# Kernel tuning notes

Hardware: AMD Instinct MI355X
Metric: run time of the kernel (lower is better)

The kernel has to match this reference:

```python
import jax, jax.numpy as jnp
import numpy as np

S, N, H = 4096, 32, 512

def setup_inputs() -> dict:
    key = jax.random.key(0)
    ks = jax.random.split(key, 8)
    scale = 1.0 / np.sqrt(H)
    return {
        "hidden": jax.random.normal(ks[0], (N, H), dtype=jnp.float32),
        "encoder_outputs": jax.random.normal(ks[1], (S, N, H), dtype=jnp.float32),
        "W_w": jax.random.uniform(ks[2], (H, H), jnp.float32, -scale, scale),
        "W_b": jax.random.uniform(ks[3], (H,), jnp.float32, -scale, scale),
        "U_w": jax.random.uniform(ks[4], (H, H), jnp.float32, -scale, scale),
        "U_b": jax.random.uniform(ks[5], (H,), jnp.float32, -scale, scale),
        "v_w": jax.random.uniform(ks[6], (1, H), jnp.float32, -scale, scale),
        "v_b": jax.random.uniform(ks[7], (1,), jnp.float32, -scale, scale),
    }

def reference(hidden, encoder_outputs, W_w, W_b, U_w, U_b, v_w, v_b):
    # W(hidden): [N,H] -> broadcast over seq dim (equivalent to expand then Linear)
    wh = hidden @ W_w.T + W_b                      # [N, H]
    ue = jnp.einsum('snh,kh->snk', encoder_outputs, U_w) + U_b  # [S, N, H]
    energy = jnp.tanh(wh[None, :, :] + ue)         # [S, N, H]
    score = jnp.einsum('snh,oh->sno', energy, v_w) + v_b        # [S, N, 1]
    attention_weights = jax.nn.softmax(score, axis=0)           # softmax over seq
    context = jnp.sum(attention_weights * encoder_outputs, axis=0)  # [N, H]
    return (context, attention_weights)
```

## Files before the change

kernel.cpp:

```cpp
#include <hip/hip_runtime.h>
#include <hip/hip_bf16.h>

#define Sdim 4096
#define Ndim 32
#define Hdim 512
#define Mdim (Sdim * Ndim)

#define BM 128
#define BN 256
#define BK 64

typedef __bf16 bf16x8 __attribute__((ext_vector_type(8)));
typedef float f32x4 __attribute__((ext_vector_type(4)));
typedef unsigned short ushort8v __attribute__((ext_vector_type(8)));

__device__ __forceinline__ void load_lds16(const void* g, void* l) {
    __builtin_amdgcn_global_load_lds(
        (const __attribute__((address_space(1))) void*)g,
        (__attribute__((address_space(3))) void*)l, 16, 0, 0);
}

__device__ __forceinline__ float ftanh(float x) {
    float e = __expf(2.f * x);
    return 1.f - 2.f / (e + 1.f);
}

__global__ __launch_bounds__(256) void k_prep_bias(
    const float* __restrict__ hidden, const float* __restrict__ Ww,
    const float* __restrict__ Wb, const float* __restrict__ Ubias,
    float* __restrict__ bias) {
    const int t = threadIdx.x, w = t >> 6, lane = t & 63;
    const int cc = blockIdx.x * 4 + w;
    const float4 w0 = *(const float4*)(Ww + (size_t)cc * Hdim + lane * 8);
    const float4 w1 = *(const float4*)(Ww + (size_t)cc * Hdim + lane * 8 + 4);
    const float wb = Wb[cc] + Ubias[cc];
    for (int n = 0; n < Ndim; ++n) {
        const float4 h0 = *(const float4*)(hidden + n * Hdim + lane * 8);
        const float4 h1 = *(const float4*)(hidden + n * Hdim + lane * 8 + 4);
        float p = w0.x * h0.x + w0.y * h0.y + w0.z * h0.z + w0.w * h0.w +
                  w1.x * h1.x + w1.y * h1.y + w1.z * h1.z + w1.w * h1.w;
        p += __shfl_xor(p, 1);  p += __shfl_xor(p, 2);
        p += __shfl_xor(p, 4);  p += __shfl_xor(p, 8);
        p += __shfl_xor(p, 16); p += __shfl_xor(p, 32);
        if (lane == 0) bias[n * Hdim + cc] = p + wb;
    }
}

__global__ __launch_bounds__(256) void k_cvt(
    const float* __restrict__ src, unsigned short* __restrict__ dst) {
    const int i = blockIdx.x * 256 + threadIdx.x;
    float4 v = ((const float4*)src)[i];
    union { __hip_bfloat162 h[2]; ushort4 u; } r;
    r.h[0] = __float22bfloat162_rn(make_float2(v.x, v.y));
    r.h[1] = __float22bfloat162_rn(make_float2(v.z, v.w));
    ((ushort4*)dst)[i] = r.u;
}

__global__ __launch_bounds__(512, 4) void k_gemm_score(
    const float* __restrict__ enc,
    const unsigned short* __restrict__ Ub,
    const float* __restrict__ bias,
    const float* __restrict__ vw,
    float* __restrict__ scorep) {
    __shared__ __align__(16) unsigned short Asm[BM][72];
    __shared__ __align__(16) unsigned short Bsm[BN * BK];
    __shared__ float ssm[4][BM];

    const int t = threadIdx.x;
    const int lane = t & 63;
    const int w = t >> 6;
    const int wM = w >> 2;
    const int wN = w & 3;
    const int c = lane & 15;
    const int q = lane >> 4;

    const int rowblk = blockIdx.x >> 1;
    const int colblk = blockIdx.x & 1;
    const int mBase = rowblk * BM;
    const int colBase = colblk * BN;

    const int ar = t >> 2;
    const int aq = t & 3;
    const int asw = ((ar >> 3) & 1) << 1;
    const float4* arow =
        (const float4*)(enc + (size_t)(mBase + ar) * Hdim) + aq * 4;
    unsigned short* awr = &Asm[ar][((2 * aq) ^ asw) * 8];

    const int coff = lane >> 3;
    const int bch = (lane & 7) ^ coff;
    const unsigned short* bsrc =
        Ub + (size_t)(colBase + w * 8 + coff) * Hdim + bch * 8;
    unsigned short* bdst = Bsm + (w * 8) * BK;

    const int sA = ((c >> 3) & 1) << 1;
    const int sB = c & 7;

    f32x4 acc[4][4];
#pragma unroll
    for (int i = 0; i < 4; ++i)
#pragma unroll
        for (int j = 0; j < 4; ++j) acc[i][j] = (f32x4){0.f, 0.f, 0.f, 0.f};

    float4 a0 = arow[0], a1 = arow[1], a2 = arow[2], a3 = arow[3];

#pragma unroll 1
    for (int kk = 0; kk < Hdim / BK; ++kk) {
        asm volatile("" ::: "memory");
        __builtin_amdgcn_s_barrier();
        asm volatile("" ::: "memory");
        __builtin_amdgcn_sched_barrier(0);

#pragma unroll
        for (int g = 0; g < 4; ++g)
            load_lds16(bsrc + (size_t)g * 64 * Hdim + kk * BK,
                       bdst + g * 64 * BK);
        asm volatile("" ::: "memory");
        __builtin_amdgcn_sched_barrier(0);

        union { __hip_bfloat162 h[4]; ushort8v v; } p0, p1;
        p0.h[0] = __float22bfloat162_rn(make_float2(a0.x, a0.y));
        p0.h[1] = __float22bfloat162_rn(make_float2(a0.z, a0.w));
        p0.h[2] = __float22bfloat162_rn(make_float2(a1.x, a1.y));
        p0.h[3] = __float22bfloat162_rn(make_float2(a1.z, a1.w));
        p1.h[0] = __float22bfloat162_rn(make_float2(a2.x, a2.y));
        p1.h[1] = __float22bfloat162_rn(make_float2(a2.z, a2.w));
        p1.h[2] = __float22bfloat162_rn(make_float2(a3.x, a3.y));
        p1.h[3] = __float22bfloat162_rn(make_float2(a3.z, a3.w));
        *(ushort8v*)awr = p0.v;
        *(ushort8v*)(awr + 8) = p1.v;

        const int kn = (kk < Hdim / BK - 1) ? kk + 1 : kk;
        const float4* ap = arow + kn * 16;
        a0 = ap[0]; a1 = ap[1]; a2 = ap[2]; a3 = ap[3];

        asm volatile("" ::: "memory");
        __builtin_amdgcn_sched_barrier(0);
        asm volatile("s_waitcnt vmcnt(4) lgkmcnt(0)" ::: "memory");
        __builtin_amdgcn_s_barrier();
        asm volatile("" ::: "memory");
        __builtin_amdgcn_sched_barrier(0);

#pragma unroll 1
        for (int h = 0; h < 2; ++h) {
            bf16x8 af[4], bfr[4];
#pragma unroll
            for (int mi = 0; mi < 4; ++mi) {
                const int row = wM * 64 + mi * 16 + c;
                af[mi] =
                    *(const bf16x8*)&Asm[row][(((h << 2) | q) ^ sA) * 8];
            }
#pragma unroll
            for (int ni = 0; ni < 4; ++ni) {
                const int lc = wN * 64 + ni * 16 + c;
                bfr[ni] = *(const bf16x8*)&Bsm[lc * BK +
                                               (((h << 2) | q) ^ sB) * 8];
            }
#pragma unroll
            for (int mi = 0; mi < 4; ++mi)
#pragma unroll
                for (int ni = 0; ni < 4; ++ni)
                    acc[mi][ni] = __builtin_amdgcn_mfma_f32_16x16x32_bf16(
                        af[mi], bfr[ni], acc[mi][ni], 0, 0, 0);
        }
    }
    asm volatile("" :: "v"(a0.x), "v"(a1.x), "v"(a2.x), "v"(a3.x));

    float vcol[4];
#pragma unroll
    for (int ni = 0; ni < 4; ++ni)
        vcol[ni] = vw[colBase + wN * 64 + ni * 16 + c];

#pragma unroll
    for (int mi = 0; mi < 4; ++mi) {
#pragma unroll
        for (int reg = 0; reg < 4; ++reg) {
            const int rl = wM * 64 + mi * 16 + q * 4 + reg;
            const int n = rl & 31;
            float p = 0.f;
#pragma unroll
            for (int ni = 0; ni < 4; ++ni) {
                const int col = colBase + wN * 64 + ni * 16 + c;
                float e = acc[mi][ni][reg] + bias[n * Hdim + col];
                p += vcol[ni] * ftanh(e);
            }
            p += __shfl_xor(p, 1);
            p += __shfl_xor(p, 2);
            p += __shfl_xor(p, 4);
            p += __shfl_xor(p, 8);
            if (c == 0) ssm[wN][rl] = p;
        }
    }
    __syncthreads();
    if (t < BM) {
        const int m = mBase + t;
        const float s = ssm[0][t] + ssm[1][t] + ssm[2][t] + ssm[3][t];
        scorep[colblk * Mdim + (m & 31) * Sdim + (m >> 5)] = s;
    }
}

__global__ __launch_bounds__(256) void k_softmax(
    const float* __restrict__ scorep,
    float* __restrict__ out_w) {
    const int n = blockIdx.x;
    const int t = threadIdx.x;
    const int w = t >> 6;
    __shared__ float row[Sdim];
    __shared__ float red[8];
    const float4* s0 = (const float4*)(scorep + n * Sdim);
    const float4* s1 = (const float4*)(scorep + Mdim + n * Sdim);

    float mx = -1e30f;
    for (int i = t; i < Sdim / 4; i += 256) {
        float4 a = s0[i], b = s1[i];
        float4 v;
        v.x = a.x + b.x; v.y = a.y + b.y; v.z = a.z + b.z; v.w = a.w + b.w;
        ((float4*)row)[i] = v;
        mx = fmaxf(mx, fmaxf(fmaxf(v.x, v.y), fmaxf(v.z, v.w)));
    }
#pragma unroll
    for (int o = 32; o > 0; o >>= 1) mx = fmaxf(mx, __shfl_xor(mx, o));
    if ((t & 63) == 0) red[w] = mx;
    __syncthreads();
    mx = fmaxf(fmaxf(red[0], red[1]), fmaxf(red[2], red[3]));

    float sum = 0.f;
    for (int i = t; i < Sdim; i += 256) sum += __expf(row[i] - mx);
#pragma unroll
    for (int o = 32; o > 0; o >>= 1) sum += __shfl_xor(sum, o);
    if ((t & 63) == 0) red[4 + w] = sum;
    __syncthreads();
    sum = red[4] + red[5] + red[6] + red[7];
    const float inv = 1.f / sum;
    for (int i = t; i < Sdim; i += 256)
        out_w[i * Ndim + n] = __expf(row[i] - mx) * inv;
}

__global__ __launch_bounds__(512) void k_context(
    const float* __restrict__ enc, const float* __restrict__ wts,
    float* __restrict__ part) {
    const int n = blockIdx.x & 31;
    const int sc = blockIdx.x >> 5;
    const int s0 = sc * 256;
    const int t = threadIdx.x;
    const int g = t >> 6;
    const int lane = t & 63;
    const int h0 = lane * 8;
    float4 c0 = {0.f, 0.f, 0.f, 0.f}, c1 = {0.f, 0.f, 0.f, 0.f};
#pragma unroll 4
    for (int it = 0; it < 32; ++it) {
        const int s = s0 + it * 8 + g;
        const float wv = wts[(size_t)s * Ndim + n];
        const float* e = enc + ((size_t)s * Ndim + n) * Hdim + h0;
        const float4 e0 = *(const float4*)e;
        const float4 e1 = *(const float4*)(e + 4);
        c0.x += wv * e0.x; c0.y += wv * e0.y;
        c0.z += wv * e0.z; c0.w += wv * e0.w;
        c1.x += wv * e1.x; c1.y += wv * e1.y;
        c1.z += wv * e1.z; c1.w += wv * e1.w;
    }
    __shared__ __align__(16) float4 red[7][128];
    if (g > 0) { red[g - 1][lane * 2] = c0; red[g - 1][lane * 2 + 1] = c1; }
    __syncthreads();
    if (g == 0) {
#pragma unroll
        for (int i = 0; i < 7; ++i) {
            const float4 b0 = red[i][lane * 2];
            const float4 b1 = red[i][lane * 2 + 1];
            c0.x += b0.x; c0.y += b0.y; c0.z += b0.z; c0.w += b0.w;
            c1.x += b1.x; c1.y += b1.y; c1.z += b1.z; c1.w += b1.w;
        }
        float* o = part + (size_t)(sc * 32 + n) * Hdim + h0;
        *(float4*)o = c0;
        *(float4*)(o + 4) = c1;
    }
}

__global__ __launch_bounds__(256) void k_ctx_reduce(
    const float* __restrict__ part, float* __restrict__ out) {
    const int j = blockIdx.x * 256 + threadIdx.x;
    float4 s = {0.f, 0.f, 0.f, 0.f};
    for (int i = 0; i < 16; ++i) {
        const float4 v = ((const float4*)part)[i * 4096 + j];
        s.x += v.x; s.y += v.y; s.z += v.z; s.w += v.w;
    }
    ((float4*)out)[j] = s;
}

extern "C" void kernel_launch(void* const* d_in, const int* in_sizes, int n_in,
                              void* d_out, int out_size, void* d_ws,
                              size_t ws_size, hipStream_t stream) {
    const float* hidden = (const float*)d_in[0];
    const float* enc    = (const float*)d_in[1];
    const float* Ww     = (const float*)d_in[2];
    const float* Wb     = (const float*)d_in[3];
    const float* Uw     = (const float*)d_in[4];
    const float* Ubias  = (const float*)d_in[5];
    const float* vw     = (const float*)d_in[6];

    float* out = (float*)d_out;

    char* ws = (char*)d_ws;
    float* bias          = (float*)(ws);
    unsigned short* Ub16 = (unsigned short*)(ws + (64 << 10));
    float* scorep        = (float*)(ws + (576 << 10));
    float* part          = (float*)(ws + (64 << 10));

    k_prep_bias<<<128, 256, 0, stream>>>(hidden, Ww, Wb, Ubias, bias);
    k_cvt<<<256, 256, 0, stream>>>(Uw, Ub16);
    k_gemm_score<<<(Mdim / BM) * 2, 512, 0, stream>>>(enc, Ub16, bias, vw,
                                                      scorep);
    k_softmax<<<Ndim, 256, 0, stream>>>(scorep, out + Ndim * Hdim);
    k_context<<<Ndim * (Sdim / 256), 512, 0, stream>>>(enc, out + Ndim * Hdim,
                                                       part);
    k_ctx_reduce<<<16, 256, 0, stream>>>(part, out);
}
```

Before: 483.1 us.

## Use full-width GEMM tiles and fuse softmax normalization into context kernel

The score GEMM now uses 64x512 tiles so each block covers all output columns. The A operand (fp32 encoder rows) is therefore read and converted once instead of twice, and the two partial-score buffers disappear. A0/A1 prefetch is double-buffered two k-steps ahead. Softmax is split: a small kernel computes 1/sum(exp(score)) with no max subtraction, and the context kernel computes and writes the normalized weights itself before the weighted sum. Dropping the max subtraction risks overflow if scores are large, and the larger B tile increases LDS use, which may reduce occupancy.

Result: slower. 495.6 us (+2.6%).

```diff
diff --git a/kernel.cpp b/kernel.cpp
--- a/kernel.cpp
+++ b/kernel.cpp
@@ -6,8 +6,8 @@
 #define Hdim 512
 #define Mdim (Sdim * Ndim)
 
-#define BM 128
-#define BN 256
+#define BM 64
+#define BN 512
 #define BK 64
 
 typedef __bf16 bf16x8 __attribute__((ext_vector_type(8)));
@@ -56,6 +56,49 @@
     ((ushort4*)dst)[i] = r.u;
 }
 
+#define GS_STEP(KK, A0, A1)                                                    \
+    {                                                                          \
+        asm volatile("" ::: "memory");                                         \
+        __builtin_amdgcn_s_barrier();                                          \
+        asm volatile("" ::: "memory");                                         \
+        __builtin_amdgcn_sched_barrier(0);                                     \
+        _Pragma("unroll") for (int g = 0; g < 8; ++g)                          \
+            load_lds16(bsrc + (size_t)g * 8 * Hdim + (KK)*BK,                  \
+                       bdst + g * 8 * BK);                                     \
+        asm volatile("" ::: "memory");                                         \
+        __builtin_amdgcn_sched_barrier(0);                                     \
+        union { __hip_bfloat162 h[4]; ushort8v v; } pk;                        \
+        pk.h[0] = __float22bfloat162_rn(make_float2(A0.x, A0.y));              \
+        pk.h[1] = __float22bfloat162_rn(make_float2(A0.z, A0.w));              \
+        pk.h[2] = __float22bfloat162_rn(make_float2(A1.x, A1.y));              \
+        pk.h[3] = __float22bfloat162_rn(make_float2(A1.z, A1.w));              \
+        *(ushort8v*)awr = pk.v;                                                \
+        {                                                                      \
+            const int kn = ((KK) + 2 < 8) ? (KK) + 2 : 7;                      \
+            A0 = *(const float4*)(abase + kn * 64);                            \
+            A1 = *(const float4*)(abase + kn * 64 + 4);                        \
+        }                                                                      \
+        asm volatile("" ::: "memory");                                         \
+        __builtin_amdgcn_sched_barrier(0);                                     \
+        asm volatile("s_waitcnt vmcnt(2) lgkmcnt(0)" ::: "memory");            \
+        __builtin_amdgcn_s_barrier();                                          \
+        asm volatile("" ::: "memory");                                         \
+        __builtin_amdgcn_sched_barrier(0);                                     \
+        _Pragma("unroll 1") for (int h = 0; h < 2; ++h) {                      \
+            bf16x8 af[4], bfr[4];                                              \
+            const int ch = (h << 2) | q;                                       \
+            _Pragma("unroll") for (int mi = 0; mi < 4; ++mi)                   \
+                af[mi] = *(const bf16x8*)&Asm[mi * 16 + c][ch * 8];            \
+            _Pragma("unroll") for (int ni = 0; ni < 4; ++ni)                   \
+                bfr[ni] = *(const bf16x8*)&Bsm[(w * 64 + ni * 16 + c) * BK +   \
+                                               ((ch ^ sB) * 8)];               \
+            _Pragma("unroll") for (int mi = 0; mi < 4; ++mi)                   \
+                _Pragma("unroll") for (int ni = 0; ni < 4; ++ni)               \
+                    acc[mi][ni] = __builtin_amdgcn_mfma_f32_16x16x32_bf16(     \
+                        af[mi], bfr[ni], acc[mi][ni], 0, 0, 0);                \
+        }                                                                      \
+    }
+
 __global__ __launch_bounds__(512, 4) void k_gemm_score(
     const float* __restrict__ enc,
     const unsigned short* __restrict__ Ub,
@@ -64,35 +107,24 @@
     float* __restrict__ scorep) {
     __shared__ __align__(16) unsigned short Asm[BM][72];
     __shared__ __align__(16) unsigned short Bsm[BN * BK];
-    __shared__ float ssm[4][BM];
+    __shared__ float ssm[8][BM];
 
     const int t = threadIdx.x;
     const int lane = t & 63;
     const int w = t >> 6;
-    const int wM = w >> 2;
-    const int wN = w & 3;
     const int c = lane & 15;
     const int q = lane >> 4;
 
-    const int rowblk = blockIdx.x >> 1;
-    const int colblk = blockIdx.x & 1;
-    const int mBase = rowblk * BM;
-    const int colBase = colblk * BN;
-
-    const int ar = t >> 2;
-    const int aq = t & 3;
-    const int asw = ((ar >> 3) & 1) << 1;
-    const float4* arow =
-        (const float4*)(enc + (size_t)(mBase + ar) * Hdim) + aq * 4;
-    unsigned short* awr = &Asm[ar][((2 * aq) ^ asw) * 8];
-
-    const int coff = lane >> 3;
-    const int bch = (lane & 7) ^ coff;
-    const unsigned short* bsrc =
-        Ub + (size_t)(colBase + w * 8 + coff) * Hdim + bch * 8;
-    unsigned short* bdst = Bsm + (w * 8) * BK;
-
-    const int sA = ((c >> 3) & 1) << 1;
+    const int mBase = blockIdx.x * BM;
+
+    const float* abase = enc + (size_t)(mBase + (t >> 3)) * Hdim + (t & 7) * 8;
+    unsigned short* awr = &Asm[t >> 3][(t & 7) * 8];
+
+    const int csub = lane >> 3;
+    const unsigned short* bsrc = Ub + (size_t)(w * 64 + csub) * Hdim +
+                                 ((lane & 7) ^ csub) * 8;
+    unsigned short* bdst = Bsm + (w * 64) * BK;
+
     const int sB = c & 7;
 
     f32x4 acc[4][4];
@@ -101,85 +133,32 @@
 #pragma unroll
         for (int j = 0; j < 4; ++j) acc[i][j] = (f32x4){0.f, 0.f, 0.f, 0.f};
 
-    float4 a0 = arow[0], a1 = arow[1], a2 = arow[2], a3 = arow[3];
+    float4 aA0 = *(const float4*)(abase + 0);
+    float4 aA1 = *(const float4*)(abase + 4);
+    float4 aB0 = *(const float4*)(abase + 64);
+    float4 aB1 = *(const float4*)(abase + 68);
 
 #pragma unroll 1
-    for (int kk = 0; kk < Hdim / BK; ++kk) {
-        asm volatile("" ::: "memory");
-        __builtin_amdgcn_s_barrier();
-        asm volatile("" ::: "memory");
-        __builtin_amdgcn_sched_barrier(0);
-
-#pragma unroll
-        for (int g = 0; g < 4; ++g)
-            load_lds16(bsrc + (size_t)g * 64 * Hdim + kk * BK,
-                       bdst + g * 64 * BK);
-        asm volatile("" ::: "memory");
-        __builtin_amdgcn_sched_barrier(0);
-
-        union { __hip_bfloat162 h[4]; ushort8v v; } p0, p1;
-        p0.h[0] = __float22bfloat162_rn(make_float2(a0.x, a0.y));
-        p0.h[1] = __float22bfloat162_rn(make_float2(a0.z, a0.w));
-        p0.h[2] = __float22bfloat162_rn(make_float2(a1.x, a1.y));
-        p0.h[3] = __float22bfloat162_rn(make_float2(a1.z, a1.w));
-        p1.h[0] = __float22bfloat162_rn(make_float2(a2.x, a2.y));
-        p1.h[1] = __float22bfloat162_rn(make_float2(a2.z, a2.w));
-        p1.h[2] = __float22bfloat162_rn(make_float2(a3.x, a3.y));
-        p1.h[3] = __float22bfloat162_rn(make_float2(a3.z, a3.w));
-        *(ushort8v*)awr = p0.v;
-        *(ushort8v*)(awr + 8) = p1.v;
-
-        const int kn = (kk < Hdim / BK - 1) ? kk + 1 : kk;
-        const float4* ap = arow + kn * 16;
-        a0 = ap[0]; a1 = ap[1]; a2 = ap[2]; a3 = ap[3];
-
-        asm volatile("" ::: "memory");
-        __builtin_amdgcn_sched_barrier(0);
-        asm volatile("s_waitcnt vmcnt(4) lgkmcnt(0)" ::: "memory");
-        __builtin_amdgcn_s_barrier();
-        asm volatile("" ::: "memory");
-        __builtin_amdgcn_sched_barrier(0);
-
-#pragma unroll 1
-        for (int h = 0; h < 2; ++h) {
-            bf16x8 af[4], bfr[4];
-#pragma unroll
-            for (int mi = 0; mi < 4; ++mi) {
-                const int row = wM * 64 + mi * 16 + c;
-                af[mi] =
-                    *(const bf16x8*)&Asm[row][(((h << 2) | q) ^ sA) * 8];
-            }
-#pragma unroll
-            for (int ni = 0; ni < 4; ++ni) {
-                const int lc = wN * 64 + ni * 16 + c;
-                bfr[ni] = *(const bf16x8*)&Bsm[lc * BK +
-                                               (((h << 2) | q) ^ sB) * 8];
-            }
-#pragma unroll
-            for (int mi = 0; mi < 4; ++mi)
-#pragma unroll
-                for (int ni = 0; ni < 4; ++ni)
-                    acc[mi][ni] = __builtin_amdgcn_mfma_f32_16x16x32_bf16(
-                        af[mi], bfr[ni], acc[mi][ni], 0, 0, 0);
-        }
-    }
-    asm volatile("" :: "v"(a0.x), "v"(a1.x), "v"(a2.x), "v"(a3.x));
+    for (int kk = 0; kk < 8; kk += 2) {
+        GS_STEP(kk, aA0, aA1);
+        GS_STEP(kk + 1, aB0, aB1);
+    }
+    asm volatile("" :: "v"(aA0.x), "v"(aA1.x), "v"(aB0.x), "v"(aB1.x));
 
     float vcol[4];
 #pragma unroll
-    for (int ni = 0; ni < 4; ++ni)
-        vcol[ni] = vw[colBase + wN * 64 + ni * 16 + c];
+    for (int ni = 0; ni < 4; ++ni) vcol[ni] = vw[w * 64 + ni * 16 + c];
 
 #pragma unroll
     for (int mi = 0; mi < 4; ++mi) {
 #pragma unroll
         for (int reg = 0; reg < 4; ++reg) {
-            const int rl = wM * 64 + mi * 16 + q * 4 + reg;
+            const int rl = mi * 16 + q * 4 + reg;
             const int n = rl & 31;
             float p = 0.f;
 #pragma unroll
             for (int ni = 0; ni < 4; ++ni) {
-                const int col = colBase + wN * 64 + ni * 16 + c;
+                const int col = w * 64 + ni * 16 + c;
                 float e = acc[mi][ni][reg] + bias[n * Hdim + col];
                 p += vcol[ni] * ftanh(e);
             }
@@ -187,56 +166,41 @@
             p += __shfl_xor(p, 2);
             p += __shfl_xor(p, 4);
             p += __shfl_xor(p, 8);
-            if (c == 0) ssm[wN][rl] = p;
+            if (c == 0) ssm[w][rl] = p;
         }
     }
     __syncthreads();
     if (t < BM) {
         const int m = mBase + t;
-        const float s = ssm[0][t] + ssm[1][t] + ssm[2][t] + ssm[3][t];
-        scorep[colblk * Mdim + (m & 31) * Sdim + (m >> 5)] = s;
-    }
-}
-
-__global__ __launch_bounds__(256) void k_softmax(
+        const float s = ssm[0][t] + ssm[1][t] + ssm[2][t] + ssm[3][t] +
+                        ssm[4][t] + ssm[5][t] + ssm[6][t] + ssm[7][t];
+        scorep[(m & 31) * Sdim + (m >> 5)] = s;
+    }
+}
+
+__global__ __launch_bounds__(256) void k_sumexp(
     const float* __restrict__ scorep,
-    float* __restrict__ out_w) {
+    float* __restrict__ sums) {
     const int n = blockIdx.x;
     const int t = threadIdx.x;
     const int w = t >> 6;
-    __shared__ float row[Sdim];
-    __shared__ float red[8];
-    const float4* s0 = (const float4*)(scorep + n * Sdim);
-    const float4* s1 = (const float4*)(scorep + Mdim + n * Sdim);
-
-    float mx = -1e30f;
+    const float4* p = (const float4*)(scorep + n * Sdim);
+    float s = 0.f;
     for (int i = t; i < Sdim / 4; i += 256) {
-        float4 a = s0[i], b = s1[i];
-        float4 v;
-        v.x = a.x + b.x; v.y = a.y + b.y; v.z = a.z + b.z; v.w = a.w + b.w;
-        ((float4*)row)[i] = v;
-        mx = fmaxf(mx, fmaxf(fmaxf(v.x, v.y), fmaxf(v.z, v.w)));
-    }
-#pragma unroll
-    for (int o = 32; o > 0; o >>= 1) mx = fmaxf(mx, __shfl_xor(mx, o));
-    if ((t & 63) == 0) red[w] = mx;
-    __syncthreads();
-    mx = fmaxf(fmaxf(red[0], red[1]), fmaxf(red[2], red[3]));
-
-    float sum = 0.f;
-    for (int i = t; i < Sdim; i += 256) sum += __expf(row[i] - mx);
-#pragma unroll
-    for (int o = 32; o > 0; o >>= 1) sum += __shfl_xor(sum, o);
-    if ((t & 63) == 0) red[4 + w] = sum;
-    __syncthreads();
-    sum = red[4] + red[5] + red[6] + red[7];
-    const float inv = 1.f / sum;
-    for (int i = t; i < Sdim; i += 256)
-        out_w[i * Ndim + n] = __expf(row[i] - mx) * inv;
+        const float4 v = p[i];
+        s += __expf(v.x) + __expf(v.y) + __expf(v.z) + __expf(v.w);
+    }
+#pragma unroll
+    for (int o = 32; o > 0; o >>= 1) s += __shfl_xor(s, o);
+    __shared__ float red[4];
+    if ((t & 63) == 0) red[w] = s;
+    __syncthreads();
+    if (t == 0) sums[n] = 1.f / (red[0] + red[1] + red[2] + red[3]);
 }
 
 __global__ __launch_bounds__(512) void k_context(
-    const float* __restrict__ enc, const float* __restrict__ wts,
+    const float* __restrict__ enc, const float* __restrict__ scorep,
+    const float* __restrict__ sums, float* __restrict__ out_w,
     float* __restrict__ part) {
     const int n = blockIdx.x & 31;
     const int sc = blockIdx.x >> 5;
@@ -245,11 +209,21 @@
     const int g = t >> 6;
     const int lane = t & 63;
     const int h0 = lane * 8;
+
+    __shared__ float wsm[256];
+    if (t < 256) {
+        const int s = s0 + t;
+        const float wv = __expf(scorep[n * Sdim + s]) * sums[n];
+        wsm[t] = wv;
+        out_w[(size_t)s * Ndim + n] = wv;
+    }
+    __syncthreads();
+
     float4 c0 = {0.f, 0.f, 0.f, 0.f}, c1 = {0.f, 0.f, 0.f, 0.f};
 #pragma unroll 4
     for (int it = 0; it < 32; ++it) {
         const int s = s0 + it * 8 + g;
-        const float wv = wts[(size_t)s * Ndim + n];
+        const float wv = wsm[it * 8 + g];
         const float* e = enc + ((size_t)s * Ndim + n) * Hdim + h0;
         const float4 e0 = *(const float4*)e;
         const float4 e1 = *(const float4*)(e + 4);
@@ -303,14 +277,14 @@
     float* bias          = (float*)(ws);
     unsigned short* Ub16 = (unsigned short*)(ws + (64 << 10));
     float* scorep        = (float*)(ws + (576 << 10));
-    float* part          = (float*)(ws + (64 << 10));
+    float* sums          = (float*)(ws + (1088 << 10));
+    float* part          = (float*)(ws + (1152 << 10));
 
     k_prep_bias<<<128, 256, 0, stream>>>(hidden, Ww, Wb, Ubias, bias);
     k_cvt<<<256, 256, 0, stream>>>(Uw, Ub16);
-    k_gemm_score<<<(Mdim / BM) * 2, 512, 0, stream>>>(enc, Ub16, bias, vw,
-                                                      scorep);
-    k_softmax<<<Ndim, 256, 0, stream>>>(scorep, out + Ndim * Hdim);
-    k_context<<<Ndim * (Sdim / 256), 512, 0, stream>>>(enc, out + Ndim * Hdim,
-                                                       part);
+    k_gemm_score<<<Mdim / BM, 512, 0, stream>>>(enc, Ub16, bias, vw, scorep);
+    k_sumexp<<<Ndim, 256, 0, stream>>>(scorep, sums);
+    k_context<<<Ndim * (Sdim / 256), 512, 0, stream>>>(enc, scorep, sums,
+                                                       out + Ndim * Hdim, part);
     k_ctx_reduce<<<16, 256, 0, stream>>>(part, out);
 }
```

## Merge prep kernels and fuse softmax normalization into context kernel

Applied to the files above, without the earlier changes.

Merges the bias precompute and weight conversion into one launch. Replaces the softmax kernel with a lighter sum-of-exponentials kernel and moves the final weight computation into the context kernel, which now writes the attention weights itself and uses half-size sequence chunks for more blocks. The max subtraction is dropped, which relies on scores staying small enough not to overflow the exponential. The partial-sum buffer doubles and the reduction loops over 32 partials.

Result: no change. 483.6 us (+0.1%).

```diff
diff --git a/kernel.cpp b/kernel.cpp
--- a/kernel.cpp
+++ b/kernel.cpp
@@ -25,35 +25,38 @@
     return 1.f - 2.f / (e + 1.f);
 }
 
-__global__ __launch_bounds__(256) void k_prep_bias(
+__global__ __launch_bounds__(256) void k_prep(
     const float* __restrict__ hidden, const float* __restrict__ Ww,
     const float* __restrict__ Wb, const float* __restrict__ Ubias,
-    float* __restrict__ bias) {
-    const int t = threadIdx.x, w = t >> 6, lane = t & 63;
-    const int cc = blockIdx.x * 4 + w;
-    const float4 w0 = *(const float4*)(Ww + (size_t)cc * Hdim + lane * 8);
-    const float4 w1 = *(const float4*)(Ww + (size_t)cc * Hdim + lane * 8 + 4);
-    const float wb = Wb[cc] + Ubias[cc];
-    for (int n = 0; n < Ndim; ++n) {
-        const float4 h0 = *(const float4*)(hidden + n * Hdim + lane * 8);
-        const float4 h1 = *(const float4*)(hidden + n * Hdim + lane * 8 + 4);
-        float p = w0.x * h0.x + w0.y * h0.y + w0.z * h0.z + w0.w * h0.w +
-                  w1.x * h1.x + w1.y * h1.y + w1.z * h1.z + w1.w * h1.w;
-        p += __shfl_xor(p, 1);  p += __shfl_xor(p, 2);
-        p += __shfl_xor(p, 4);  p += __shfl_xor(p, 8);
-        p += __shfl_xor(p, 16); p += __shfl_xor(p, 32);
-        if (lane == 0) bias[n * Hdim + cc] = p + wb;
-    }
-}
-
-__global__ __launch_bounds__(256) void k_cvt(
-    const float* __restrict__ src, unsigned short* __restrict__ dst) {
-    const int i = blockIdx.x * 256 + threadIdx.x;
-    float4 v = ((const float4*)src)[i];
-    union { __hip_bfloat162 h[2]; ushort4 u; } r;
-    r.h[0] = __float22bfloat162_rn(make_float2(v.x, v.y));
-    r.h[1] = __float22bfloat162_rn(make_float2(v.z, v.w));
-    ((ushort4*)dst)[i] = r.u;
+    float* __restrict__ bias, const float* __restrict__ Uw,
+    unsigned short* __restrict__ Ub16) {
+    const int t = threadIdx.x;
+    if (blockIdx.x < 128) {
+        const int w = t >> 6, lane = t & 63;
+        const int cc = blockIdx.x * 4 + w;
+        const float4 w0 = *(const float4*)(Ww + (size_t)cc * Hdim + lane * 8);
+        const float4 w1 =
+            *(const float4*)(Ww + (size_t)cc * Hdim + lane * 8 + 4);
+        const float wb = Wb[cc] + Ubias[cc];
+        for (int n = 0; n < Ndim; ++n) {
+            const float4 h0 = *(const float4*)(hidden + n * Hdim + lane * 8);
+            const float4 h1 =
+                *(const float4*)(hidden + n * Hdim + lane * 8 + 4);
+            float p = w0.x * h0.x + w0.y * h0.y + w0.z * h0.z + w0.w * h0.w +
+                      w1.x * h1.x + w1.y * h1.y + w1.z * h1.z + w1.w * h1.w;
+            p += __shfl_xor(p, 1);  p += __shfl_xor(p, 2);
+            p += __shfl_xor(p, 4);  p += __shfl_xor(p, 8);
+            p += __shfl_xor(p, 16); p += __shfl_xor(p, 32);
+            if (lane == 0) bias[n * Hdim + cc] = p + wb;
+        }
+    } else {
+        const int i = (blockIdx.x - 128) * 256 + t;
+        float4 v = ((const float4*)Uw)[i];
+        union { __hip_bfloat162 h[2]; ushort4 u; } r;
+        r.h[0] = __float22bfloat162_rn(make_float2(v.x, v.y));
+        r.h[1] = __float22bfloat162_rn(make_float2(v.z, v.w));
+        ((ushort4*)Ub16)[i] = r.u;
+    }
 }
 
 __global__ __launch_bounds__(512, 4) void k_gemm_score(
@@ -101,7 +104,10 @@
 #pragma unroll
         for (int j = 0; j < 4; ++j) acc[i][j] = (f32x4){0.f, 0.f, 0.f, 0.f};
 
-    float4 a0 = arow[0], a1 = arow[1], a2 = arow[2], a3 = arow[3];
+    float4 a0 = *(const float4*)(arow + 0);
+    float4 a1 = *(const float4*)(arow + 1);
+    float4 a2 = *(const float4*)(arow + 2);
+    float4 a3 = *(const float4*)(arow + 3);
 
 #pragma unroll 1
     for (int kk = 0; kk < Hdim / BK; ++kk) {
@@ -198,58 +204,55 @@
     }
 }
 
-__global__ __launch_bounds__(256) void k_softmax(
+__global__ __launch_bounds__(256) void k_sumexp(
     const float* __restrict__ scorep,
-    float* __restrict__ out_w) {
+    float* __restrict__ sums) {
     const int n = blockIdx.x;
     const int t = threadIdx.x;
     const int w = t >> 6;
-    __shared__ float row[Sdim];
-    __shared__ float red[8];
-    const float4* s0 = (const float4*)(scorep + n * Sdim);
-    const float4* s1 = (const float4*)(scorep + Mdim + n * Sdim);
-
-    float mx = -1e30f;
+    const float4* p0 = (const float4*)(scorep + n * Sdim);
+    const float4* p1 = (const float4*)(scorep + Mdim + n * Sdim);
+    float s = 0.f;
     for (int i = t; i < Sdim / 4; i += 256) {
-        float4 a = s0[i], b = s1[i];
-        float4 v;
-        v.x = a.x + b.x; v.y = a.y + b.y; v.z = a.z + b.z; v.w = a.w + b.w;
-        ((float4*)row)[i] = v;
-        mx = fmaxf(mx, fmaxf(fmaxf(v.x, v.y), fmaxf(v.z, v.w)));
-    }
-#pragma unroll
-    for (int o = 32; o > 0; o >>= 1) mx = fmaxf(mx, __shfl_xor(mx, o));
-    if ((t & 63) == 0) red[w] = mx;
+        const float4 a = p0[i], b = p1[i];
+        s += __expf(a.x + b.x) + __expf(a.y + b.y) + __expf(a.z + b.z) +
+             __expf(a.w + b.w);
+    }
+#pragma unroll
+    for (int o = 32; o > 0; o >>= 1) s += __shfl_xor(s, o);
+    __shared__ float red[4];
+    if ((t & 63) == 0) red[w] = s;
     __syncthreads();
-    mx = fmaxf(fmaxf(red[0], red[1]), fmaxf(red[2], red[3]));
-
-    float sum = 0.f;
-    for (int i = t; i < Sdim; i += 256) sum += __expf(row[i] - mx);
-#pragma unroll
-    for (int o = 32; o > 0; o >>= 1) sum += __shfl_xor(sum, o);
-    if ((t & 63) == 0) red[4 + w] = sum;
-    __syncthreads();
-    sum = red[4] + red[5] + red[6] + red[7];
-    const float inv = 1.f / sum;
-    for (int i = t; i < Sdim; i += 256)
-        out_w[i * Ndim + n] = __expf(row[i] - mx) * inv;
+    if (t == 0) sums[n] = 1.f / (red[0] + red[1] + red[2] + red[3]);
 }
 
 __global__ __launch_bounds__(512) void k_context(
-    const float* __restrict__ enc, const float* __restrict__ wts,
+    const float* __restrict__ enc, const float* __restrict__ scorep,
+    const float* __restrict__ sums, float* __restrict__ out_w,
     float* __restrict__ part) {
     const int n = blockIdx.x & 31;
     const int sc = blockIdx.x >> 5;
-    const int s0 = sc * 256;
+    const int s0 = sc * 128;
     const int t = threadIdx.x;
     const int g = t >> 6;
     const int lane = t & 63;
     const int h0 = lane * 8;
+
+    __shared__ float wsm[128];
+    if (t < 128) {
+        const int s = s0 + t;
+        const float sv = scorep[n * Sdim + s] + scorep[Mdim + n * Sdim + s];
+        const float wv = __expf(sv) * sums[n];
+        wsm[t] = wv;
+        out_w[(size_t)s * Ndim + n] = wv;
+    }
+    __syncthreads();
+
     float4 c0 = {0.f, 0.f, 0.f, 0.f}, c1 = {0.f, 0.f, 0.f, 0.f};
 #pragma unroll 4
-    for (int it = 0; it < 32; ++it) {
+    for (int it = 0; it < 16; ++it) {
         const int s = s0 + it * 8 + g;
-        const float wv = wts[(size_t)s * Ndim + n];
+        const float wv = wsm[it * 8 + g];
         const float* e = enc + ((size_t)s * Ndim + n) * Hdim + h0;
         const float4 e0 = *(const float4*)e;
         const float4 e1 = *(const float4*)(e + 4);
@@ -279,7 +282,7 @@
     const float* __restrict__ part, float* __restrict__ out) {
     const int j = blockIdx.x * 256 + threadIdx.x;
     float4 s = {0.f, 0.f, 0.f, 0.f};
-    for (int i = 0; i < 16; ++i) {
+    for (int i = 0; i < 32; ++i) {
         const float4 v = ((const float4*)part)[i * 4096 + j];
         s.x += v.x; s.y += v.y; s.z += v.z; s.w += v.w;
     }
@@ -303,14 +306,14 @@
     float* bias          = (float*)(ws);
     unsigned short* Ub16 = (unsigned short*)(ws + (64 << 10));
     float* scorep        = (float*)(ws + (576 << 10));
-    float* part          = (float*)(ws + (64 << 10));
-
-    k_prep_bias<<<128, 256, 0, stream>>>(hidden, Ww, Wb, Ubias, bias);
-    k_cvt<<<256, 256, 0, stream>>>(Uw, Ub16);
+    float* sums          = (float*)(ws + (1600 << 10));
+    float* part          = (float*)(ws + (1664 << 10));
+
+    k_prep<<<384, 256, 0, stream>>>(hidden, Ww, Wb, Ubias, bias, Uw, Ub16);
     k_gemm_score<<<(Mdim / BM) * 2, 512, 0, stream>>>(enc, Ub16, bias, vw,
                                                       scorep);
-    k_softmax<<<Ndim, 256, 0, stream>>>(scorep, out + Ndim * Hdim);
-    k_context<<<Ndim * (Sdim / 256), 512, 0, stream>>>(enc, out + Ndim * Hdim,
-                                                       part);
+    k_sumexp<<<Ndim, 256, 0, stream>>>(scorep, sums);
+    k_context<<<Ndim * (Sdim / 128), 512, 0, stream>>>(enc, scorep, sums,
+                                                       out + Ndim * Hdim, part);
     k_ctx_reduce<<<16, 256, 0, stream>>>(part, out);
 }
```
